# Kernel tuning notes

Hardware: AMD Instinct MI355X
Metric: run time of the kernel (lower is better)

## Reference

```python
import jax, jax.numpy as jnp
import numpy as np

B = 4096
SEQ = 128            # window_size * rnn_in_pkts
WINDOW = 32
IN_PKTS = 4
LEN_V, LEN_E = 1500, 64
IPD_V, IPD_E = 256, 64
EV = 64              # embedding_vector_bits
RNN_IN = IN_PKTS * EV   # 256
H = 256              # rnn_hidden_bits
LABELS = 100


def setup_inputs() -> dict:
    key = jax.random.key(0)
    ks = jax.random.split(key, 12)
    s = 0.05
    return {
        "len_x": jax.random.randint(ks[0], (B, SEQ), 0, LEN_V),
        "ipd_x": jax.random.randint(ks[1], (B, SEQ), 0, IPD_V),
        "len_emb": jax.random.normal(ks[2], (LEN_V, LEN_E), jnp.float32) * s,
        "ipd_emb": jax.random.normal(ks[3], (IPD_V, IPD_E), jnp.float32) * s,
        "fc_w": jax.random.normal(ks[4], (EV, LEN_E + IPD_E), jnp.float32) * s,
        "fc_b": jax.random.normal(ks[5], (EV,), jnp.float32) * s,
        "w_ih": jax.random.normal(ks[6], (3 * H, RNN_IN), jnp.float32) * s,
        "w_hh": jax.random.normal(ks[7], (3 * H, H), jnp.float32) * s,
        "b_ih": jax.random.normal(ks[8], (3 * H,), jnp.float32) * s,
        "b_hh": jax.random.normal(ks[9], (3 * H,), jnp.float32) * s,
        "out_w": jax.random.normal(ks[10], (LABELS, H), jnp.float32) * s,
        "out_b": jax.random.normal(ks[11], (LABELS,), jnp.float32) * s,
    }


def _gru_scan(rnn_in, w_ih, w_hh, b_ih, b_hh):
    # rnn_in: [B, T, RNN_IN]. Precompute input-side gates for all steps at once.
    gi_all = jnp.einsum("bti,gi->btg", rnn_in, w_ih) + b_ih  # [B,T,3H]
    h0 = jnp.zeros((rnn_in.shape[0], H), rnn_in.dtype)

    def step(h, gi):
        gh = h @ w_hh.T + b_hh                 # [B,3H]
        i_r, i_z, i_n = jnp.split(gi, 3, axis=-1)
        h_r, h_z, h_n = jnp.split(gh, 3, axis=-1)
        r = jax.nn.sigmoid(i_r + h_r)
        z = jax.nn.sigmoid(i_z + h_z)
        n = jnp.tanh(i_n + r * h_n)
        h_new = (1.0 - z) * n + z * h
        return h_new, None

    h_final, _ = jax.lax.scan(step, h0, jnp.swapaxes(gi_all, 0, 1))
    return h_final


def reference(len_x, ipd_x, len_emb, ipd_emb, fc_w, fc_b, w_ih, w_hh, b_ih, b_hh, out_w, out_b):
    len_e = len_emb[len_x]                      # [B,SEQ,LEN_E]
    ipd_e = ipd_emb[ipd_x]                      # [B,SEQ,IPD_E]
    cat = jnp.concatenate([len_e, ipd_e], axis=-1)
    evs = cat @ fc_w.T + fc_b                   # [B,SEQ,EV]
    rnn_in = evs.reshape(B, WINDOW, RNN_IN)     # [B,32,256]
    h = _gru_scan(rnn_in, w_ih, w_hh, b_ih, b_hh)
    logits = h @ out_w.T + out_b                # [B,LABELS]
    return logits
```

## Files before the change

### kernel.cpp

```cpp
#include <hip/hip_runtime.h>
#include <hip/hip_bf16.h>

typedef __bf16 bf16_t;
typedef __bf16 bf16x8 __attribute__((ext_vector_type(8)));
typedef float f32x4 __attribute__((ext_vector_type(4)));
typedef unsigned short u16x4 __attribute__((ext_vector_type(4)));

#define MFMA16(a, b, c) __builtin_amdgcn_mfma_f32_16x16x32_bf16((a), (b), (c), 0, 0, 0)

#define BATCH 4096
#define SEQN 128
#define HN 256
#define NLABELS 100
#define TSTEPS 32
#define LEN_VN 1500
#define IPD_VN 256

#define OFF_LENT   0u
#define OFF_IPDT   384000u
#define OFF_WIH    449536u
#define OFF_WHH    842752u
#define OFF_GI     1235968u
#define WS_NEEDED  202562560u

__device__ __forceinline__ float sigf(float x) {
    return __builtin_amdgcn_rcpf(1.f + __expf(-x));
}
__device__ __forceinline__ float tanh_fast(float x) {
    return 2.f * __builtin_amdgcn_rcpf(1.f + __expf(-2.f * x)) - 1.f;
}
__device__ __forceinline__ float b2f(unsigned short v) {
    union { unsigned u; float f; } c; c.u = ((unsigned)v) << 16; return c.f;
}
__device__ __forceinline__ unsigned short f2b(float f) {
    union { bf16_t h; unsigned short s; } c; c.h = (bf16_t)f; return c.s;
}

__device__ __forceinline__ void barrier_lds() {
    asm volatile("s_waitcnt lgkmcnt(0)\n\ts_barrier" ::: "memory");
}

__global__ void prep_kernel(const float* __restrict__ len_emb,
                            const float* __restrict__ ipd_emb,
                            const float* __restrict__ fc_w,
                            const float* __restrict__ fc_b,
                            const float* __restrict__ w_ih,
                            const float* __restrict__ w_hh,
                            float* __restrict__ lenT, float* __restrict__ ipdT,
                            bf16_t* __restrict__ wfrag_ih,
                            bf16_t* __restrict__ wfrag_hh) {
    const int bid = blockIdx.x, tid = threadIdx.x;
    if (bid < 439) {
        const int row = bid * 4 + (tid >> 6);
        const int e = tid & 63;
        if (row < LEN_VN) {
            const float* emb = len_emb + row * 64;
            const float* wv = fc_w + e * 128;
            float s = fc_b[e];
            #pragma unroll 8
            for (int j = 0; j < 64; ++j) s += emb[j] * wv[j];
            lenT[row * 64 + e] = s;
        } else if (row < LEN_VN + IPD_VN) {
            const int v = row - LEN_VN;
            const float* emb = ipd_emb + v * 64;
            const float* wv = fc_w + e * 128 + 64;
            float s = 0.f;
            #pragma unroll 8
            for (int j = 0; j < 64; ++j) s += emb[j] * wv[j];
            ipdT[v * 64 + e] = s;
        }
    } else {
        const int flat = (bid - 439) * 256 + tid;
        const int which = flat / 24576;
        const int rem = flat % 24576;
        const int c = rem >> 9;
        const int kt = (rem >> 6) & 7;
        const int lane = rem & 63;
        const int g = c * 16 + (lane & 15);
        const int k0 = kt * 32 + (lane >> 4) * 8;
        const float* src = (which == 0 ? w_ih : w_hh) + g * 256 + k0;
        bf16_t* dst = (which == 0 ? wfrag_ih : wfrag_hh) + ((c * 8 + kt) * 64 + lane) * 8;
        f32x4 s0 = *(const f32x4*)(src);
        f32x4 s1 = *(const f32x4*)(src + 4);
        bf16x8 o;
        #pragma unroll
        for (int j = 0; j < 4; ++j) { o[j] = (bf16_t)s0[j]; o[4 + j] = (bf16_t)s1[j]; }
        *(bf16x8*)dst = o;
    }
}

__global__ void __launch_bounds__(512, 2)
gemm_gi(const int* __restrict__ len_x, const int* __restrict__ ipd_x,
        const float* __restrict__ lenT, const float* __restrict__ ipdT,
        const bf16_t* __restrict__ wfrag_ih,
        const float* __restrict__ b_ih, const float* __restrict__ b_hh,
        bf16_t* __restrict__ gi) {
    __shared__ bf16_t wlds[8 * 8 * 512];
    __shared__ bf16_t a_lds[2][8 * 512];

    const int tid = threadIdx.x;
    const int lane = tid & 63;
    const int w = tid >> 6;
    const int bt = blockIdx.x;
    const int quad = lane >> 4;

    const int cts[6] = {2*w, 2*w + 1, 16 + 2*w, 17 + 2*w, 32 + 2*w, 33 + 2*w};

    bf16x8 wr[5][8];
    #pragma unroll
    for (int cc = 0; cc < 5; ++cc)
        #pragma unroll
        for (int kt = 0; kt < 8; ++kt)
            wr[cc][kt] = *(const bf16x8*)(wfrag_ih + ((cts[cc] * 8 + kt) * 64 + lane) * 8);
    #pragma unroll
    for (int kt = 0; kt < 8; ++kt)
        *(bf16x8*)&wlds[(w * 8 + kt) * 512 + lane * 8] =
            *(const bf16x8*)(wfrag_ih + ((cts[5] * 8 + kt) * 64 + lane) * 8);

    f32x4 bias[6];
    #pragma unroll
    for (int cc = 0; cc < 6; ++cc) {
        f32x4 v = *(const f32x4*)(b_ih + cts[cc] * 16 + quad * 4);
        if (cc < 4) v += *(const f32x4*)(b_hh + cts[cc] * 16 + quad * 4);
        bias[cc] = v;
    }

    const int b_row = bt * 16 + (lane & 15);
    const int k0 = w * 32 + quad * 8;
    const int p = k0 >> 6;
    const int e0 = k0 & 63;

    auto do_gather = [&](int t) {
        const int seq = t * 4 + p;
        const int v1 = len_x[b_row * SEQN + seq];
        const int v2 = ipd_x[b_row * SEQN + seq];
        const f32x4* lp = (const f32x4*)(lenT + v1 * 64 + e0);
        const f32x4* ip = (const f32x4*)(ipdT + v2 * 64 + e0);
        f32x4 a0 = lp[0] + ip[0];
        f32x4 a1 = lp[1] + ip[1];
        bf16x8 o;
        #pragma unroll
        for (int j = 0; j < 4; ++j) { o[j] = (bf16_t)a0[j]; o[4 + j] = (bf16_t)a1[j]; }
        *(bf16x8*)&a_lds[t & 1][w * 512 + lane * 8] = o;
    };

    do_gather(0);
    bf16_t* gib = gi + (size_t)bt * 48 * 32 * 256 + lane * 4;
    const bf16_t* wb = &wlds[w * 8 * 512 + lane * 8];

    for (int t = 0; t < TSTEPS; ++t) {
        barrier_lds();
        if (t + 1 < TSTEPS) do_gather(t + 1);

        f32x4 acc[6] = {};
        const bf16_t* ab = &a_lds[t & 1][lane * 8];
        #pragma unroll
        for (int kt = 0; kt < 8; ++kt) {
            bf16x8 xf = *(const bf16x8*)(ab + kt * 512);
            bf16x8 w5 = *(const bf16x8*)(wb + kt * 512);
            acc[0] = MFMA16(wr[0][kt], xf, acc[0]);
            acc[1] = MFMA16(wr[1][kt], xf, acc[1]);
            acc[2] = MFMA16(wr[2][kt], xf, acc[2]);
            acc[3] = MFMA16(wr[3][kt], xf, acc[3]);
            acc[4] = MFMA16(wr[4][kt], xf, acc[4]);
            acc[5] = MFMA16(w5, xf, acc[5]);
        }

        #pragma unroll
        for (int cc = 0; cc < 6; ++cc) {
            u16x4 o;
            #pragma unroll
            for (int r = 0; r < 4; ++r) o[r] = f2b(acc[cc][r] + bias[cc][r]);
            *(u16x4*)(gib + ((size_t)cts[cc] * 32 + t) * 256) = o;
        }
    }
}

__global__ void __launch_bounds__(512, 2)
gru_kernel(const bf16_t* __restrict__ gi,
           const bf16_t* __restrict__ wfrag_hh,
           const float* __restrict__ b_hh,
           const float* __restrict__ out_w,
           const float* __restrict__ out_b,
           float* __restrict__ out) {
    __shared__ char smem[81920];
    bf16_t* wlds = (bf16_t*)smem;
    bf16_t* h_lds = (bf16_t*)(smem + 65536);
    float* h_fin = (float*)smem;

    const int tid = threadIdx.x;
    const int lane = tid & 63;
    const int w = tid >> 6;
    const int bt = blockIdx.x;
    const int quad = lane >> 4;
    const int b = lane & 15;

    const int cts[6] = {2*w, 2*w + 1, 16 + 2*w, 17 + 2*w, 32 + 2*w, 33 + 2*w};

    bf16x8 wr[5][8];
    #pragma unroll
    for (int cc = 0; cc < 5; ++cc)
        #pragma unroll
        for (int kt = 0; kt < 8; ++kt)
            wr[cc][kt] = *(const bf16x8*)(wfrag_hh + ((cts[cc] * 8 + kt) * 64 + lane) * 8);
    #pragma unroll
    for (int kt = 0; kt < 8; ++kt)
        *(bf16x8*)&wlds[(w * 8 + kt) * 512 + lane * 8] =
            *(const bf16x8*)(wfrag_hh + ((cts[5] * 8 + kt) * 64 + lane) * 8);

    f32x4 bhn[2];
    bhn[0] = *(const f32x4*)(b_hh + cts[4] * 16 + quad * 4);
    bhn[1] = *(const f32x4*)(b_hh + cts[5] * 16 + quad * 4);

    for (int i = tid; i < 4096; i += 512) h_lds[4096 + i] = (bf16_t)0.f;

    int woff[2];
    #pragma unroll
    for (int s = 0; s < 2; ++s)
        woff[s] = w * 512 + (((2 * s + (quad >> 1)) & 3) * 16 + b) * 8 + 4 * (quad & 1);

    f32x4 hprev[2] = {};
    const bf16_t* gib = gi + (size_t)bt * 48 * 32 * 256 + lane * 4;
    const bf16_t* wb = &wlds[w * 8 * 512 + lane * 8];

    for (int t = 0; t < TSTEPS; ++t) {
        barrier_lds();

        u16x4 g[6];
        #pragma unroll
        for (int cc = 0; cc < 6; ++cc)
            g[cc] = *(const u16x4*)(gib + ((size_t)cts[cc] * 32 + t) * 256);

        const bf16_t* hb = &h_lds[((t + 1) & 1) * 4096 + lane * 8];
        f32x4 acc[6] = {};
        #pragma unroll
        for (int kt = 0; kt < 8; ++kt) {
            bf16x8 hf = *(const bf16x8*)(hb + kt * 512);
            bf16x8 w5 = *(const bf16x8*)(wb + kt * 512);
            acc[0] = MFMA16(wr[0][kt], hf, acc[0]);
            acc[1] = MFMA16(wr[1][kt], hf, acc[1]);
            acc[2] = MFMA16(wr[2][kt], hf, acc[2]);
            acc[3] = MFMA16(wr[3][kt], hf, acc[3]);
            acc[4] = MFMA16(wr[4][kt], hf, acc[4]);
            acc[5] = MFMA16(w5, hf, acc[5]);
        }

        bf16_t* hwb = &h_lds[(t & 1) * 4096];
        #pragma unroll
        for (int s = 0; s < 2; ++s) {
            u16x4 o;
            #pragma unroll
            for (int r = 0; r < 4; ++r) {
                float rg = sigf(acc[s][r] + b2f(g[s][r]));
                float zg = sigf(acc[2 + s][r] + b2f(g[2 + s][r]));
                float ng = tanh_fast(b2f(g[4 + s][r]) + rg * (acc[4 + s][r] + bhn[s][r]));
                float hn = ng + zg * (hprev[s][r] - ng);
                hprev[s][r] = hn;
                o[r] = f2b(hn);
            }
            *(u16x4*)(hwb + woff[s]) = o;
        }
    }

    __syncthreads();

    #pragma unroll
    for (int s = 0; s < 2; ++s)
        *(f32x4*)(h_fin + b * 260 + 32 * w + 16 * s + 4 * quad) = hprev[s];
    __syncthreads();

    for (int i = tid; i < 16 * NLABELS; i += 512) {
        const int row = i / NLABELS;
        const int cl = i - row * NLABELS;
        const f32x4* wrow = (const f32x4*)(out_w + cl * 256);
        const f32x4* hr = (const f32x4*)(h_fin + row * 260);
        f32x4 acc = {0.f, 0.f, 0.f, 0.f};
        #pragma unroll 4
        for (int k = 0; k < 64; ++k) acc += hr[k] * wrow[k];
        out[(bt * 16 + row) * NLABELS + cl] =
            out_b[cl] + acc[0] + acc[1] + acc[2] + acc[3];
    }
}

extern "C" void kernel_launch(void* const* d_in, const int* in_sizes, int n_in,
                              void* d_out, int out_size, void* d_ws, size_t ws_size,
                              hipStream_t stream) {
    (void)in_sizes; (void)n_in; (void)out_size; (void)ws_size;
    const int*   len_x   = (const int*)d_in[0];
    const int*   ipd_x   = (const int*)d_in[1];
    const float* len_emb = (const float*)d_in[2];
    const float* ipd_emb = (const float*)d_in[3];
    const float* fc_w    = (const float*)d_in[4];
    const float* fc_b    = (const float*)d_in[5];
    const float* w_ih    = (const float*)d_in[6];
    const float* w_hh    = (const float*)d_in[7];
    const float* b_ih    = (const float*)d_in[8];
    const float* b_hh    = (const float*)d_in[9];
    const float* out_w   = (const float*)d_in[10];
    const float* out_b   = (const float*)d_in[11];

    char* ws = (char*)d_ws;
    float*  lenT = (float*)(ws + OFF_LENT);
    float*  ipdT = (float*)(ws + OFF_IPDT);
    bf16_t* wfi  = (bf16_t*)(ws + OFF_WIH);
    bf16_t* wfh  = (bf16_t*)(ws + OFF_WHH);
    bf16_t* gi   = (bf16_t*)(ws + OFF_GI);

    prep_kernel<<<631, 256, 0, stream>>>(len_emb, ipd_emb, fc_w, fc_b,
                                         w_ih, w_hh, lenT, ipdT, wfi, wfh);
    gemm_gi<<<256, 512, 0, stream>>>(len_x, ipd_x, lenT, ipdT, wfi,
                                     b_ih, b_hh, gi);
    gru_kernel<<<256, 512, 0, stream>>>(gi, wfh, b_hh, out_w, out_b,
                                        (float*)d_out);
}
```

Measured before the change: 263.9 us.

## Split GRU recurrence across 16 waves and prefetch input gates

After: 234.4 us. 11.2% less time.

```diff
diff --git a/kernel.cpp b/kernel.cpp
--- a/kernel.cpp
+++ b/kernel.cpp
@@ -21,7 +21,6 @@
 #define OFF_WIH    449536u
 #define OFF_WHH    842752u
 #define OFF_GI     1235968u
-#define WS_NEEDED  202562560u
 
 __device__ __forceinline__ float sigf(float x) {
     return __builtin_amdgcn_rcpf(1.f + __expf(-x));
@@ -31,6 +30,12 @@
 }
 __device__ __forceinline__ float b2f(unsigned short v) {
     union { unsigned u; float f; } c; c.u = ((unsigned)v) << 16; return c.f;
+}
+__device__ __forceinline__ f32x4 b2f4(u16x4 v) {
+    f32x4 o;
+    #pragma unroll
+    for (int r = 0; r < 4; ++r) o[r] = b2f(v[r]);
+    return o;
 }
 __device__ __forceinline__ unsigned short f2b(float f) {
     union { bf16_t h; unsigned short s; } c; c.h = (bf16_t)f; return c.s;
@@ -125,23 +130,26 @@
         bias[cc] = v;
     }
 
-    const int b_row = bt * 16 + (lane & 15);
-    const int k0 = w * 32 + quad * 8;
-    const int p = k0 >> 6;
-    const int e0 = k0 & 63;
+    const int pair = tid >> 3;
+    const int sub = tid & 7;
+    const int grow = pair & 15;
+    const int p = pair >> 4;
+    const int e0 = sub * 8;
+    const int b_row = bt * 16 + grow;
+    const int goff = (2 * p + (sub >> 2)) * 512 + ((sub & 3) * 16 + grow) * 8;
 
     auto do_gather = [&](int t) {
         const int seq = t * 4 + p;
         const int v1 = len_x[b_row * SEQN + seq];
         const int v2 = ipd_x[b_row * SEQN + seq];
-        const f32x4* lp = (const f32x4*)(lenT + v1 * 64 + e0);
-        const f32x4* ip = (const f32x4*)(ipdT + v2 * 64 + e0);
-        f32x4 a0 = lp[0] + ip[0];
-        f32x4 a1 = lp[1] + ip[1];
+        const float* lp = lenT + v1 * 64 + e0;
+        const float* ip = ipdT + v2 * 64 + e0;
+        f32x4 a0 = *(const f32x4*)lp + *(const f32x4*)ip;
+        f32x4 a1 = *(const f32x4*)(lp + 4) + *(const f32x4*)(ip + 4);
         bf16x8 o;
         #pragma unroll
         for (int j = 0; j < 4; ++j) { o[j] = (bf16_t)a0[j]; o[4 + j] = (bf16_t)a1[j]; }
-        *(bf16x8*)&a_lds[t & 1][w * 512 + lane * 8] = o;
+        *(bf16x8*)&a_lds[t & 1][goff] = o;
     };
 
     do_gather(0);
@@ -152,7 +160,10 @@
         barrier_lds();
         if (t + 1 < TSTEPS) do_gather(t + 1);
 
-        f32x4 acc[6] = {};
+        f32x4 acc[6];
+        #pragma unroll
+        for (int cc = 0; cc < 6; ++cc) acc[cc] = bias[cc];
+
         const bf16_t* ab = &a_lds[t & 1][lane * 8];
         #pragma unroll
         for (int kt = 0; kt < 8; ++kt) {
@@ -170,22 +181,22 @@
         for (int cc = 0; cc < 6; ++cc) {
             u16x4 o;
             #pragma unroll
-            for (int r = 0; r < 4; ++r) o[r] = f2b(acc[cc][r] + bias[cc][r]);
+            for (int r = 0; r < 4; ++r) o[r] = f2b(acc[cc][r]);
             *(u16x4*)(gib + ((size_t)cts[cc] * 32 + t) * 256) = o;
         }
     }
 }
 
-__global__ void __launch_bounds__(512, 2)
+__global__ void __launch_bounds__(1024, 4)
 gru_kernel(const bf16_t* __restrict__ gi,
            const bf16_t* __restrict__ wfrag_hh,
            const float* __restrict__ b_hh,
            const float* __restrict__ out_w,
            const float* __restrict__ out_b,
            float* __restrict__ out) {
-    __shared__ char smem[81920];
+    __shared__ char smem[147456];
     bf16_t* wlds = (bf16_t*)smem;
-    bf16_t* h_lds = (bf16_t*)(smem + 65536);
+    bf16_t* h_lds = (bf16_t*)(smem + 131072);
     float* h_fin = (float*)smem;
 
     const int tid = threadIdx.x;
@@ -195,81 +206,81 @@
     const int quad = lane >> 4;
     const int b = lane & 15;
 
-    const int cts[6] = {2*w, 2*w + 1, 16 + 2*w, 17 + 2*w, 32 + 2*w, 33 + 2*w};
-
-    bf16x8 wr[5][8];
-    #pragma unroll
-    for (int cc = 0; cc < 5; ++cc)
+    bf16x8 wr[2][8];
+    #pragma unroll
+    for (int cc = 0; cc < 2; ++cc) {
+        const int ct = cc * 16 + w;
         #pragma unroll
         for (int kt = 0; kt < 8; ++kt)
-            wr[cc][kt] = *(const bf16x8*)(wfrag_hh + ((cts[cc] * 8 + kt) * 64 + lane) * 8);
+            wr[cc][kt] = *(const bf16x8*)(wfrag_hh + ((ct * 8 + kt) * 64 + lane) * 8);
+    }
     #pragma unroll
     for (int kt = 0; kt < 8; ++kt)
         *(bf16x8*)&wlds[(w * 8 + kt) * 512 + lane * 8] =
-            *(const bf16x8*)(wfrag_hh + ((cts[5] * 8 + kt) * 64 + lane) * 8);
-
-    f32x4 bhn[2];
-    bhn[0] = *(const f32x4*)(b_hh + cts[4] * 16 + quad * 4);
-    bhn[1] = *(const f32x4*)(b_hh + cts[5] * 16 + quad * 4);
-
-    for (int i = tid; i < 4096; i += 512) h_lds[4096 + i] = (bf16_t)0.f;
-
-    int woff[2];
-    #pragma unroll
-    for (int s = 0; s < 2; ++s)
-        woff[s] = w * 512 + (((2 * s + (quad >> 1)) & 3) * 16 + b) * 8 + 4 * (quad & 1);
-
-    f32x4 hprev[2] = {};
+            *(const bf16x8*)(wfrag_hh + (((32 + w) * 8 + kt) * 64 + lane) * 8);
+
+    const f32x4 bhn = *(const f32x4*)(b_hh + (32 + w) * 16 + quad * 4);
+
+    for (int i = tid; i < 4096; i += 1024) h_lds[4096 + i] = (bf16_t)0.f;
+
+    const int j0 = 16 * w + 4 * quad;
+    const int woff = (j0 >> 5) * 512 + ((((j0 >> 3) & 3)) * 16 + b) * 8 + (j0 & 7);
+
     const bf16_t* gib = gi + (size_t)bt * 48 * 32 * 256 + lane * 4;
     const bf16_t* wb = &wlds[w * 8 * 512 + lane * 8];
 
+    u16x4 gc0 = *(const u16x4*)(gib + ((size_t)(w) * 32) * 256);
+    u16x4 gc1 = *(const u16x4*)(gib + ((size_t)(16 + w) * 32) * 256);
+    u16x4 gc2 = *(const u16x4*)(gib + ((size_t)(32 + w) * 32) * 256);
+
+    f32x4 hprev = {};
+
     for (int t = 0; t < TSTEPS; ++t) {
         barrier_lds();
 
-        u16x4 g[6];
-        #pragma unroll
-        for (int cc = 0; cc < 6; ++cc)
-            g[cc] = *(const u16x4*)(gib + ((size_t)cts[cc] * 32 + t) * 256);
+        f32x4 acc0 = b2f4(gc0);
+        f32x4 acc1 = b2f4(gc1);
+        f32x4 acc2 = bhn;
+        u16x4 g2cur = gc2;
+
+        if (t + 1 < TSTEPS) {
+            gc0 = *(const u16x4*)(gib + ((size_t)(w) * 32 + t + 1) * 256);
+            gc1 = *(const u16x4*)(gib + ((size_t)(16 + w) * 32 + t + 1) * 256);
+            gc2 = *(const u16x4*)(gib + ((size_t)(32 + w) * 32 + t + 1) * 256);
+        }
 
         const bf16_t* hb = &h_lds[((t + 1) & 1) * 4096 + lane * 8];
-        f32x4 acc[6] = {};
         #pragma unroll
         for (int kt = 0; kt < 8; ++kt) {
             bf16x8 hf = *(const bf16x8*)(hb + kt * 512);
             bf16x8 w5 = *(const bf16x8*)(wb + kt * 512);
-            acc[0] = MFMA16(wr[0][kt], hf, acc[0]);
-            acc[1] = MFMA16(wr[1][kt], hf, acc[1]);
-            acc[2] = MFMA16(wr[2][kt], hf, acc[2]);
-            acc[3] = MFMA16(wr[3][kt], hf, acc[3]);
-            acc[4] = MFMA16(wr[4][kt], hf, acc[4]);
-            acc[5] = MFMA16(w5, hf, acc[5]);
-        }
-
-        bf16_t* hwb = &h_lds[(t & 1) * 4096];
-        #pragma unroll
-        for (int s = 0; s < 2; ++s) {
-            u16x4 o;
-            #pragma unroll
-            for (int r = 0; r < 4; ++r) {
-                float rg = sigf(acc[s][r] + b2f(g[s][r]));
-                float zg = sigf(acc[2 + s][r] + b2f(g[2 + s][r]));
-                float ng = tanh_fast(b2f(g[4 + s][r]) + rg * (acc[4 + s][r] + bhn[s][r]));
-                float hn = ng + zg * (hprev[s][r] - ng);
-                hprev[s][r] = hn;
-                o[r] = f2b(hn);
-            }
-            *(u16x4*)(hwb + woff[s]) = o;
-        }
+            acc0 = MFMA16(wr[0][kt], hf, acc0);
+            acc1 = MFMA16(wr[1][kt], hf, acc1);
+            acc2 = MFMA16(w5, hf, acc2);
+        }
+
+        f32x4 rg, zg;
+        #pragma unroll
+        for (int r = 0; r < 4; ++r) { rg[r] = sigf(acc0[r]); zg[r] = sigf(acc1[r]); }
+        f32x4 u = b2f4(g2cur) + rg * acc2;
+        f32x4 ng;
+        #pragma unroll
+        for (int r = 0; r < 4; ++r) ng[r] = tanh_fast(u[r]);
+        f32x4 hn = ng + zg * (hprev - ng);
+        hprev = hn;
+
+        u16x4 o;
+        #pragma unroll
+        for (int r = 0; r < 4; ++r) o[r] = f2b(hn[r]);
+        *(u16x4*)(&h_lds[(t & 1) * 4096 + woff]) = o;
     }
 
     __syncthreads();
 
-    #pragma unroll
-    for (int s = 0; s < 2; ++s)
-        *(f32x4*)(h_fin + b * 260 + 32 * w + 16 * s + 4 * quad) = hprev[s];
+    *(f32x4*)(h_fin + b * 260 + j0) = hprev;
     __syncthreads();
 
-    for (int i = tid; i < 16 * NLABELS; i += 512) {
+    for (int i = tid; i < 16 * NLABELS; i += 1024) {
         const int row = i / NLABELS;
         const int cl = i - row * NLABELS;
         const f32x4* wrow = (const f32x4*)(out_w + cl * 256);
@@ -310,6 +321,6 @@
                                          w_ih, w_hh, lenT, ipdT, wfi, wfh);
     gemm_gi<<<256, 512, 0, stream>>>(len_x, ipd_x, lenT, ipdT, wfi,
                                      b_ih, b_hh, gi);
-    gru_kernel<<<256, 512, 0, stream>>>(gi, wfh, b_hh, out_w, out_b,
-                                        (float*)d_out);
-}
+    gru_kernel<<<256, 1024, 0, stream>>>(gi, wfh, b_hh, out_w, out_b,
+                                         (float*)d_out);
+}
```
